# Performance work log

Measured on AMD Instinct MI355X. Metric: run time of the kernel, lower is better.

Reference implementation:

```python
import jax, jax.numpy as jnp
import numpy as np

TEMPERATURE = 0.07
NEG_INF = -1e9  # mask value safe for fp16/bf16 softmax


def setup_inputs() -> dict:
    key = jax.random.key(0)
    features = jax.random.normal(key, (8192, 128), dtype=jnp.float32)
    return {"features": features}


def reference(features):
    # L2-normalize rows
    f = features / jnp.linalg.norm(features, axis=1, keepdims=True)
    n = f.shape[0]          # 2 * batch_size
    b = n // 2
    # [n, n] cosine similarity / temperature
    sim = jnp.matmul(f, f.T) / TEMPERATURE
    idx = jnp.arange(n)
    # positive pair index: i <-> i + b (mod n)
    pos = sim[idx, (idx + b) % n]
    # Per row i, CE with the positive as class 0 over [pos, negatives].
    # Denominator = exp(pos) + sum(negatives) = sum over all j != i,
    # so mask only the diagonal and take a row logsumexp.
    sim_masked = jnp.where(jnp.eye(n, dtype=bool), NEG_INF, sim)
    lse = jax.nn.logsumexp(sim_masked, axis=1)
    return jnp.mean(lse - pos)
```

## Files before the change

### kernel.cpp

```cpp
#include <hip/hip_runtime.h>
#include <hip/hip_bf16.h>
#include <stdint.h>


#define N_ROWS 8192
#define DIM    128
#define HALF_N 4096
#define N_SLICES 16
#define JCOLS (N_ROWS / N_SLICES)
#define CHUNK 128
#define NCHUNK (JCOLS / CHUNK)
#define NJT (CHUNK / 16)

static constexpr float INV_T = 14.285714285714286f;
static constexpr float SCALE = 20.60992915555662f;

typedef __attribute__((ext_vector_type(8))) short short8;
typedef __attribute__((ext_vector_type(4))) float f32x4;

#if __has_builtin(__builtin_amdgcn_exp2f)
__device__ inline float fast_exp2(float x) { return __builtin_amdgcn_exp2f(x); }
#else
__device__ inline float fast_exp2(float x) { return exp2f(x); }
#endif

__device__ inline float bf_lo(uint32_t u) { return __uint_as_float(u << 16); }
__device__ inline float bf_hi(uint32_t u) { return __uint_as_float(u & 0xFFFF0000u); }
__device__ inline uint16_t f2bf(float x) {
    uint32_t u = __float_as_uint(x);
    return (uint16_t)((u + 0x7FFFu + ((u >> 16) & 1u)) >> 16);
}

__device__ inline void load_lds16(const void* g, void* l) {
    __builtin_amdgcn_global_load_lds(
        (const __attribute__((address_space(1))) uint32_t*)g,
        (__attribute__((address_space(3))) uint32_t*)l, 16, 0, 0);
}

__global__ __launch_bounds__(256) void k_normalize(const float* __restrict__ f,
                                                   uint16_t* __restrict__ fn) {
    int wid  = (blockIdx.x * blockDim.x + threadIdx.x) >> 6;
    int lane = threadIdx.x & 63;
    const float2* src = (const float2*)(f + (size_t)wid * DIM);
    float2 v = src[lane];
    float ss = v.x * v.x + v.y * v.y;
    #pragma unroll
    for (int m = 1; m < 64; m <<= 1) ss += __shfl_xor(ss, m, 64);
    float inv = rsqrtf(ss);
    ushort2 o;
    o.x = f2bf(v.x * inv);
    o.y = f2bf(v.y * inv);
    ((ushort2*)(fn + (size_t)wid * DIM))[lane] = o;
}

__global__ __launch_bounds__(256) void k_simexp(const uint16_t* __restrict__ fn,
                                                float* __restrict__ E_part) {
    __shared__ __align__(16) uint16_t Bl[2][CHUNK * DIM];
    const int tid  = threadIdx.x;
    const int lane = tid & 63;
    const int w    = tid >> 6;
    const int ib   = blockIdx.x * 256 + w * 64;
    const int jc0  = blockIdx.y * JCOLS;
    const int lr = lane & 15;
    const int lk = lane >> 4;

    const short8* fn8 = (const short8*)fn;

    short8 Af[4][4];
    #pragma unroll
    for (int mt = 0; mt < 4; ++mt)
        #pragma unroll
        for (int kc = 0; kc < 4; ++kc)
            Af[mt][kc] = fn8[(size_t)(ib + mt * 16 + lr) * 16 + kc * 4 + lk];

    float es[4][4];
    #pragma unroll
    for (int mt = 0; mt < 4; ++mt)
        #pragma unroll
        for (int r = 0; r < 4; ++r) es[mt][r] = 0.0f;

    const int scc0 = w * 32 + (lane >> 4);
    #define STAGE(c, buf)                                                     \
        _Pragma("unroll")                                                     \
        for (int i = 0; i < 8; ++i) {                                         \
            int cc = scc0 + i * 4;                                            \
            int lc = (lane & 15) ^ (cc & 7);                                  \
            load_lds16(fn8 + (size_t)(jc0 + (c) * CHUNK + cc) * 16 + lc,      \
                       &Bl[buf][w * 4096 + i * 512]);                         \
        }

    STAGE(0, 0)

    for (int c = 0; c < NCHUNK; ++c) {
        __syncthreads();
        if (c + 1 < NCHUNK) {
            STAGE(c + 1, (c + 1) & 1)
        }
        const char* bp = (const char*)&Bl[c & 1][0];
        #pragma unroll
        for (int jt = 0; jt < NJT; ++jt) {
            const int rbase = (jt * 16 + lr) * 256;
            short8 Bf[4];
            #pragma unroll
            for (int kc = 0; kc < 4; ++kc)
                Bf[kc] = *(const short8*)(bp + rbase + ((((kc << 2) | lk) ^ (lr & 7)) << 4));
            #pragma unroll
            for (int mt = 0; mt < 4; ++mt) {
                f32x4 acc = {0.0f, 0.0f, 0.0f, 0.0f};
                #pragma unroll
                for (int kc = 0; kc < 4; ++kc)
                    acc = __builtin_amdgcn_mfma_f32_16x16x32_bf16(Af[mt][kc], Bf[kc], acc, 0, 0, 0);
                #pragma unroll
                for (int r = 0; r < 4; ++r)
                    es[mt][r] += fast_exp2(fmaf(acc[r], SCALE, -SCALE));
            }
        }
    }

    #pragma unroll
    for (int mt = 0; mt < 4; ++mt)
        #pragma unroll
        for (int r = 0; r < 4; ++r) {
            float v = es[mt][r];
            v += __shfl_xor(v, 1, 64);
            v += __shfl_xor(v, 2, 64);
            v += __shfl_xor(v, 4, 64);
            v += __shfl_xor(v, 8, 64);
            if (lr == 0)
                E_part[(size_t)(ib + mt * 16 + lk * 4 + r) * N_SLICES + blockIdx.y] = v;
        }
}

__global__ __launch_bounds__(256) void k_finalize(const uint16_t* __restrict__ fn,
                                                  const float* __restrict__ E_part,
                                                  float* __restrict__ terms) {
    __shared__ float sm[4];
    int wid  = (blockIdx.x * blockDim.x + threadIdx.x) >> 6;
    int lane = threadIdx.x & 63;
    int partner = (wid + HALF_N) & (N_ROWS - 1);
    const uint32_t* fr = (const uint32_t*)(fn + (size_t)wid * DIM);
    const uint32_t* pr = (const uint32_t*)(fn + (size_t)partner * DIM);
    uint32_t a = fr[lane], p = pr[lane];
    float a0 = bf_lo(a), a1 = bf_hi(a);
    float p0 = bf_lo(p), p1 = bf_hi(p);
    float sd = a0 * a0 + a1 * a1;
    float pd = a0 * p0 + a1 * p1;
    #pragma unroll
    for (int m = 1; m < 64; m <<= 1) {
        sd += __shfl_xor(sd, m, 64);
        pd += __shfl_xor(pd, m, 64);
    }
    float e = (lane < N_SLICES) ? E_part[(size_t)wid * N_SLICES + lane] : 0.0f;
    #pragma unroll
    for (int m = 1; m < 64; m <<= 1) e += __shfl_xor(e, m, 64);
    if (lane == 0) {
        float ep = e - fast_exp2(fmaf(sd, SCALE, -SCALE));
        sm[threadIdx.x >> 6] = INV_T + logf(ep) - pd * INV_T;
    }
    __syncthreads();
    if (threadIdx.x == 0)
        terms[blockIdx.x] = sm[0] + sm[1] + sm[2] + sm[3];
}

__global__ __launch_bounds__(256) void k_reduce(const float* __restrict__ terms,
                                                float* __restrict__ out) {
    __shared__ float sm[4];
    float acc = 0.0f;
    for (int i = threadIdx.x; i < N_ROWS / 4; i += 256) acc += terms[i];
    #pragma unroll
    for (int m = 1; m < 64; m <<= 1) acc += __shfl_xor(acc, m, 64);
    if ((threadIdx.x & 63) == 0) sm[threadIdx.x >> 6] = acc;
    __syncthreads();
    if (threadIdx.x == 0)
        out[0] = (sm[0] + sm[1] + sm[2] + sm[3]) * (1.0f / N_ROWS);
}

extern "C" void kernel_launch(void* const* d_in, const int* in_sizes, int n_in,
                              void* d_out, int out_size, void* d_ws, size_t ws_size,
                              hipStream_t stream) {
    const float* feat = (const float*)d_in[0];
    float* out = (float*)d_out;

    uint16_t* fn  = (uint16_t*)d_ws;
    float* E_part = (float*)((char*)d_ws + (size_t)N_ROWS * DIM * 2);
    float* terms  = E_part + (size_t)N_ROWS * N_SLICES;

    k_normalize<<<dim3(N_ROWS / 4), dim3(256), 0, stream>>>(feat, fn);
    k_simexp<<<dim3(N_ROWS / 256, N_SLICES), dim3(256), 0, stream>>>(fn, E_part);
    k_finalize<<<dim3(N_ROWS / 4), dim3(256), 0, stream>>>(fn, E_part, terms);
    k_reduce<<<dim3(1), dim3(256), 0, stream>>>(terms, out);
}
```

Before: 45.93 us.

## Exploit symmetry of similarity matrix with upper-triangular tiles and atomic column sums

The similarity matrix is symmetric, so only upper-triangular 256x256 tiles are computed. Each off-diagonal tile adds its exp values to both its row sums and its column sums through float atomics, which roughly halves the MFMA and exp work. The per-slice partial buffer is replaced by a single accumulator vector that the normalize kernel zeroes. The cost is many global atomics per tile, a nondeterministic summation order, and fewer blocks (528 instead of 512 with less work each), which may leave the GPU less well occupied.

```diff
diff --git a/kernel.cpp b/kernel.cpp
--- a/kernel.cpp
+++ b/kernel.cpp
@@ -6,11 +6,12 @@
 #define N_ROWS 8192
 #define DIM    128
 #define HALF_N 4096
-#define N_SLICES 16
-#define JCOLS (N_ROWS / N_SLICES)
-#define CHUNK 128
-#define NCHUNK (JCOLS / CHUNK)
-#define NJT (CHUNK / 16)
+#define NBANDS 32
+#define BROWS  256
+#define NTRI   (NBANDS * (NBANDS + 1) / 2)
+#define CHUNK  128
+#define NCH    (BROWS / CHUNK)
+#define NJT    (CHUNK / 16)
 
 static constexpr float INV_T = 14.285714285714286f;
 static constexpr float SCALE = 20.60992915555662f;
@@ -38,7 +39,14 @@
 }
 
 __global__ __launch_bounds__(256) void k_normalize(const float* __restrict__ f,
-                                                   uint16_t* __restrict__ fn) {
+                                                   uint16_t* __restrict__ fn,
+                                                   float* __restrict__ E) {
+    if (blockIdx.x == 0) {
+        float4 z = {0.f, 0.f, 0.f, 0.f};
+        #pragma unroll
+        for (int i = 0; i < 8; ++i)
+            ((float4*)E)[threadIdx.x + i * 256] = z;
+    }
     int wid  = (blockIdx.x * blockDim.x + threadIdx.x) >> 6;
     int lane = threadIdx.x & 63;
     const float2* src = (const float2*)(f + (size_t)wid * DIM);
@@ -54,13 +62,18 @@
 }
 
 __global__ __launch_bounds__(256) void k_simexp(const uint16_t* __restrict__ fn,
-                                                float* __restrict__ E_part) {
+                                                float* __restrict__ E) {
     __shared__ __align__(16) uint16_t Bl[2][CHUNK * DIM];
+    int bx = 0, rem = blockIdx.x;
+    while (rem >= NBANDS - bx) { rem -= NBANDS - bx; ++bx; }
+    const int by = bx + rem;
+    const bool diag = (by == bx);
+
     const int tid  = threadIdx.x;
     const int lane = tid & 63;
     const int w    = tid >> 6;
-    const int ib   = blockIdx.x * 256 + w * 64;
-    const int jc0  = blockIdx.y * JCOLS;
+    const int ib   = bx * BROWS + w * 64;
+    const int jb   = by * BROWS;
     const int lr = lane & 15;
     const int lk = lane >> 4;
 
@@ -85,15 +98,15 @@
         for (int i = 0; i < 8; ++i) {                                         \
             int cc = scc0 + i * 4;                                            \
             int lc = (lane & 15) ^ (cc & 7);                                  \
-            load_lds16(fn8 + (size_t)(jc0 + (c) * CHUNK + cc) * 16 + lc,      \
+            load_lds16(fn8 + (size_t)(jb + (c) * CHUNK + cc) * 16 + lc,       \
                        &Bl[buf][w * 4096 + i * 512]);                         \
         }
 
     STAGE(0, 0)
 
-    for (int c = 0; c < NCHUNK; ++c) {
+    for (int c = 0; c < NCH; ++c) {
         __syncthreads();
-        if (c + 1 < NCHUNK) {
+        if (c + 1 < NCH) {
             STAGE(c + 1, (c + 1) & 1)
         }
         const char* bp = (const char*)&Bl[c & 1][0];
@@ -104,6 +117,7 @@
             #pragma unroll
             for (int kc = 0; kc < 4; ++kc)
                 Bf[kc] = *(const short8*)(bp + rbase + ((((kc << 2) | lk) ^ (lr & 7)) << 4));
+            float cs = 0.0f;
             #pragma unroll
             for (int mt = 0; mt < 4; ++mt) {
                 f32x4 acc = {0.0f, 0.0f, 0.0f, 0.0f};
@@ -111,8 +125,17 @@
                 for (int kc = 0; kc < 4; ++kc)
                     acc = __builtin_amdgcn_mfma_f32_16x16x32_bf16(Af[mt][kc], Bf[kc], acc, 0, 0, 0);
                 #pragma unroll
-                for (int r = 0; r < 4; ++r)
-                    es[mt][r] += fast_exp2(fmaf(acc[r], SCALE, -SCALE));
+                for (int r = 0; r < 4; ++r) {
+                    float e = fast_exp2(fmaf(acc[r], SCALE, -SCALE));
+                    es[mt][r] += e;
+                    cs += e;
+                }
+            }
+            if (!diag) {
+                cs += __shfl_xor(cs, 16, 64);
+                cs += __shfl_xor(cs, 32, 64);
+                if (lk == 0)
+                    atomicAdd(&E[jb + c * CHUNK + jt * 16 + lr], cs);
             }
         }
     }
@@ -127,12 +150,12 @@
             v += __shfl_xor(v, 4, 64);
             v += __shfl_xor(v, 8, 64);
             if (lr == 0)
-                E_part[(size_t)(ib + mt * 16 + lk * 4 + r) * N_SLICES + blockIdx.y] = v;
+                atomicAdd(&E[ib + mt * 16 + lk * 4 + r], v);
         }
 }
 
 __global__ __launch_bounds__(256) void k_finalize(const uint16_t* __restrict__ fn,
-                                                  const float* __restrict__ E_part,
+                                                  const float* __restrict__ E,
                                                   float* __restrict__ terms) {
     __shared__ float sm[4];
     int wid  = (blockIdx.x * blockDim.x + threadIdx.x) >> 6;
@@ -150,11 +173,8 @@
         sd += __shfl_xor(sd, m, 64);
         pd += __shfl_xor(pd, m, 64);
     }
-    float e = (lane < N_SLICES) ? E_part[(size_t)wid * N_SLICES + lane] : 0.0f;
-    #pragma unroll
-    for (int m = 1; m < 64; m <<= 1) e += __shfl_xor(e, m, 64);
     if (lane == 0) {
-        float ep = e - fast_exp2(fmaf(sd, SCALE, -SCALE));
+        float ep = E[wid] - fast_exp2(fmaf(sd, SCALE, -SCALE));
         sm[threadIdx.x >> 6] = INV_T + logf(ep) - pd * INV_T;
     }
     __syncthreads();
@@ -181,12 +201,12 @@
     const float* feat = (const float*)d_in[0];
     float* out = (float*)d_out;
 
-    uint16_t* fn  = (uint16_t*)d_ws;
-    float* E_part = (float*)((char*)d_ws + (size_t)N_ROWS * DIM * 2);
-    float* terms  = E_part + (size_t)N_ROWS * N_SLICES;
-
-    k_normalize<<<dim3(N_ROWS / 4), dim3(256), 0, stream>>>(feat, fn);
-    k_simexp<<<dim3(N_ROWS / 256, N_SLICES), dim3(256), 0, stream>>>(fn, E_part);
-    k_finalize<<<dim3(N_ROWS / 4), dim3(256), 0, stream>>>(fn, E_part, terms);
+    uint16_t* fn = (uint16_t*)d_ws;
+    float* E     = (float*)((char*)d_ws + (size_t)N_ROWS * DIM * 2);
+    float* terms = E + N_ROWS;
+
+    k_normalize<<<dim3(N_ROWS / 4), dim3(256), 0, stream>>>(feat, fn, E);
+    k_simexp<<<dim3(NTRI), dim3(256), 0, stream>>>(fn, E);
+    k_finalize<<<dim3(N_ROWS / 4), dim3(256), 0, stream>>>(fn, E, terms);
     k_reduce<<<dim3(1), dim3(256), 0, stream>>>(terms, out);
 }
```

Result: slower. 51.52 us (+12.2%).
